# Kernel tuning notes

Hardware: AMD Instinct MI355X
Metric: run time of the kernel (lower is better)

Reference implementation:

```python
import jax, jax.numpy as jnp
import numpy as np

EPS = 0.1        # entropic regularization
MAX_ITER = 50    # max Sinkhorn iterations
THRESH = 0.1     # early-stop threshold on |u - u1|


def setup_inputs() -> dict:
    key = jax.random.key(0)
    kx, ky = jax.random.split(key)
    x = jax.random.normal(kx, (4, 3072, 32), dtype=jnp.float32)
    y = jax.random.normal(ky, (4, 3072, 32), dtype=jnp.float32)
    return {"x": x, "y": y}


def _sinkhorn(x, y):
    B, P1, _ = x.shape
    P2 = y.shape[1]
    x2 = jnp.sum(x * x, axis=-1)                       # [B, P1]
    y2 = jnp.sum(y * y, axis=-1)                       # [B, P2]
    C = x2[:, :, None] + y2[:, None, :] - 2.0 * jnp.einsum('bid,bjd->bij', x, y)  # [B,P1,P2]

    log_mu = jnp.log(jnp.float32(1.0 / P1) + 1e-8)     # uniform marginals
    log_nu = jnp.log(jnp.float32(1.0 / P2) + 1e-8)

    def M(u, v):
        # modified cost M_ij = (-C_ij + u_i + v_j) / eps
        return (-C + u[:, :, None] + v[:, None, :]) / EPS

    def step(carry, _):
        u, v, done = carry
        u_new = EPS * (log_mu - jax.nn.logsumexp(M(u, v), axis=-1)) + u
        v_new = EPS * (log_nu - jax.nn.logsumexp(M(u_new, v), axis=-2)) + v
        err = jnp.mean(jnp.sum(jnp.abs(u_new - u), axis=-1))
        # freeze updates once converged (emulates the torch early break)
        u_out = jnp.where(done, u, u_new)
        v_out = jnp.where(done, v, v_new)
        done = done | (err < THRESH)
        return (u_out, v_out, done), None

    u0 = jnp.zeros((B, P1), dtype=C.dtype)
    v0 = jnp.zeros((B, P2), dtype=C.dtype)
    (u, v, _), _ = jax.lax.scan(jax.checkpoint(step), (u0, v0, jnp.array(False)),
                                None, length=MAX_ITER)

    pi = jnp.exp(M(u, v))                              # transport plan [B,P1,P2]
    cost = jnp.sum(pi * C, axis=(-2, -1))              # [B]  (reduction='none')
    return cost, pi, C


def reference(x, y):
    return _sinkhorn(x, y)
```

## Files before the change

kernel.cpp:

```cpp
#include <hip/hip_runtime.h>
#include <math.h>

#define BATCH 4
#define P 3072
#define NROW (BATCH * P)
#define NTILE (NROW / 16)
#define TPB (P / 16)
#define MAXIT 50
#define LSE_GRID NTILE

#define LN2 0.69314718055994531f
#define INV_LN2 1.44269504088896341f

typedef _Float16 f16x8 __attribute__((ext_vector_type(8)));
typedef float f32x4 __attribute__((ext_vector_type(4)));

__device__ inline float waveReduceSum(float v) {
#pragma unroll
  for (int off = 32; off > 0; off >>= 1) v += __shfl_xor(v, off, 64);
  return v;
}
__device__ inline float fexp2(float x) { return __builtin_amdgcn_exp2f(x); }
__device__ inline float flog2(float x) { return __builtin_amdgcn_logf(x); }

__global__ __launch_bounds__(256) void prep_kernel(const float* __restrict__ x,
                                                   const float* __restrict__ y,
                                                   _Float16* __restrict__ xh,
                                                   _Float16* __restrict__ yh,
                                                   float* __restrict__ x2,
                                                   float* __restrict__ y2,
                                                   float* __restrict__ vb) {
  int t = threadIdx.x;
  int lane = t & 63;
  int g = lane >> 4, r = lane & 15;
  int tileG = blockIdx.x * 4 + (t >> 6);
  int isY = tileG >= NTILE;
  int tile = isY ? (tileG - NTILE) : tileG;
  const float* src = isY ? y : x;
  int row = tile * 16 + r;
  const float* p = src + (size_t)row * 32 + g * 8;
  float4 v0 = *(const float4*)p;
  float4 v1 = *(const float4*)(p + 4);
  float sq = v0.x * v0.x + v0.y * v0.y + v0.z * v0.z + v0.w * v0.w +
             v1.x * v1.x + v1.y * v1.y + v1.z * v1.z + v1.w * v1.w;
  sq += __shfl_xor(sq, 16, 64);
  sq += __shfl_xor(sq, 32, 64);
  float scale = isY ? 1.0f : 20.0f * INV_LN2;
  f16x8 h;
  h[0] = (_Float16)(scale * v0.x); h[1] = (_Float16)(scale * v0.y);
  h[2] = (_Float16)(scale * v0.z); h[3] = (_Float16)(scale * v0.w);
  h[4] = (_Float16)(scale * v1.x); h[5] = (_Float16)(scale * v1.y);
  h[6] = (_Float16)(scale * v1.z); h[7] = (_Float16)(scale * v1.w);
  _Float16* dst = (isY ? yh : xh) + (size_t)tile * 512 + lane * 8;
  *(f16x8*)dst = h;
  if (lane < 16) {
    if (isY) { y2[row] = sq; vb[row] = -10.0f * INV_LN2 * sq; }
    else     { x2[row] = sq; }
  }
}

template <int PASS>
__global__ __launch_bounds__(256) void lse_kernel(const _Float16* __restrict__ A16,
                                                  const _Float16* __restrict__ B16,
                                                  const float* __restrict__ biasIn,
                                                  const float* __restrict__ nrm,
                                                  float* __restrict__ pot,
                                                  float* __restrict__ biasOut,
                                                  float* __restrict__ errpart,
                                                  int* __restrict__ done_arr,
                                                  int it, float lmn) {
  int tid = threadIdx.x;
  if (done_arr[it]) {
    if (PASS == 1 && blockIdx.x == 0 && tid == 0) done_arr[it + 1] = 1;
    return;
  }
  int lane = tid & 63;
  int w = tid >> 6;
  int rsel = lane & 15;
  int b = blockIdx.x / TPB;
  f16x8 afr = *(const f16x8*)(A16 + (size_t)blockIdx.x * 512 + lane * 8);
  int jt0 = b * TPB + w * 48;
  const _Float16* Bp = B16 + (size_t)jt0 * 512 + lane * 8;
  const float* biasp = biasIn + b * P + w * 768 + rsel;
  float m[4], s[4];
#pragma unroll
  for (int r = 0; r < 4; ++r) { m[r] = -1e30f; s[r] = 0.f; }
#pragma unroll 3
  for (int c = 0; c < 12; ++c) {
    f16x8 bfr[4];
    float bb[4];
#pragma unroll
    for (int t4 = 0; t4 < 4; ++t4) {
      bfr[t4] = *(const f16x8*)(Bp + ((size_t)(c * 4 + t4) << 9));
      bb[t4] = biasp[(c * 4 + t4) * 16];
    }
    f32x4 acc[4];
#pragma unroll
    for (int t4 = 0; t4 < 4; ++t4) {
      f32x4 ci = {bb[t4], bb[t4], bb[t4], bb[t4]};
      acc[t4] = __builtin_amdgcn_mfma_f32_16x16x32_f16(afr, bfr[t4], ci, 0, 0, 0);
    }
#pragma unroll
    for (int r = 0; r < 4; ++r) {
      float a0 = acc[0][r], a1 = acc[1][r], a2 = acc[2][r], a3 = acc[3][r];
      float cm = fmaxf(fmaxf(a0, a1), fmaxf(a2, a3));
      float nm = fmaxf(m[r], cm);
      float e = fexp2(a0 - nm) + fexp2(a1 - nm) + fexp2(a2 - nm) + fexp2(a3 - nm);
      s[r] = s[r] * fexp2(m[r] - nm) + e;
      m[r] = nm;
    }
  }
#pragma unroll
  for (int r = 0; r < 4; ++r) {
#pragma unroll
    for (int off = 1; off < 16; off <<= 1) {
      float om = __shfl_xor(m[r], off, 64);
      float os = __shfl_xor(s[r], off, 64);
      float nm = fmaxf(m[r], om);
      s[r] = s[r] * fexp2(m[r] - nm) + os * fexp2(om - nm);
      m[r] = nm;
    }
  }
  __shared__ float lm[4][16], ls[4][16];
  if (rsel == 0) {
    int g = lane >> 4;
#pragma unroll
    for (int r = 0; r < 4; ++r) {
      lm[w][g * 4 + r] = m[r];
      ls[w][g * 4 + r] = s[r];
    }
  }
  __syncthreads();
  float e = 0.f;
  if (tid < 16) {
    float M = lm[0][tid], S = ls[0][tid];
#pragma unroll
    for (int w2 = 1; w2 < 4; ++w2) {
      float om = lm[w2][tid], os = ls[w2][tid];
      float nm = fmaxf(M, om);
      S = S * fexp2(M - nm) + os * fexp2(om - nm);
      M = nm;
    }
    float L2v = M + flog2(S);
    int gi = blockIdx.x * 16 + tid;
    float nv = 0.1f * lmn + nrm[gi] - 0.1f * LN2 * L2v;
    if (PASS == 0) e = fabsf(nv - pot[gi]);
    pot[gi] = nv;
    biasOut[gi] = 10.0f * INV_LN2 * (nv - nrm[gi]);
  }
  if (PASS == 0) {
    if (tid < 64) {
      e = waveReduceSum(e);
      if (tid == 0) errpart[blockIdx.x] = e;
    }
  } else if (blockIdx.x == 0) {
    __shared__ float rr[4];
    float ts = 0.f;
    for (int q = tid; q < LSE_GRID; q += 256) ts += errpart[q];
    ts = waveReduceSum(ts);
    if ((tid & 63) == 0) rr[tid >> 6] = ts;
    __syncthreads();
    if (tid == 0)
      done_arr[it + 1] = ((rr[0] + rr[1] + rr[2] + rr[3]) * 0.25f < 0.1f) ? 1 : 0;
  }
}

__global__ __launch_bounds__(256) void final_kernel(const float* __restrict__ x,
                                                    const float* __restrict__ y,
                                                    const float* __restrict__ x2,
                                                    const float* __restrict__ y2,
                                                    const float* __restrict__ u,
                                                    const float* __restrict__ v,
                                                    float* __restrict__ C,
                                                    float* __restrict__ pi,
                                                    float* __restrict__ costpart) {
  __shared__ float xs[64][33];
  __shared__ float ys[64][33];
  int t = threadIdx.x;
  int b = blockIdx.z;
  int i0 = blockIdx.x * 64;
  int j0 = blockIdx.y * 64;
  const float4* xg = (const float4*)(x + ((size_t)b * P + i0) * 32);
  const float4* yg = (const float4*)(y + ((size_t)b * P + j0) * 32);
#pragma unroll
  for (int k = 0; k < 2; ++k) {
    int f4 = t + k * 256;
    int row = f4 >> 3;
    int col = (f4 & 7) << 2;
    float4 xv = xg[f4];
    xs[row][col] = xv.x; xs[row][col + 1] = xv.y; xs[row][col + 2] = xv.z; xs[row][col + 3] = xv.w;
    float4 yv = yg[f4];
    ys[row][col] = yv.x; ys[row][col + 1] = yv.y; ys[row][col + 2] = yv.z; ys[row][col + 3] = yv.w;
  }
  __syncthreads();
  int ti = t >> 4, tj = t & 15;
  int ib = ti * 4, jb = tj * 4;
  float acc[4][4];
#pragma unroll
  for (int a = 0; a < 4; ++a)
#pragma unroll
    for (int bb = 0; bb < 4; ++bb) acc[a][bb] = 0.f;
#pragma unroll 8
  for (int k = 0; k < 32; ++k) {
    float xa[4], yb[4];
#pragma unroll
    for (int a = 0; a < 4; ++a) xa[a] = xs[ib + a][k];
#pragma unroll
    for (int bb = 0; bb < 4; ++bb) yb[bb] = ys[jb + bb][k];
#pragma unroll
    for (int a = 0; a < 4; ++a)
#pragma unroll
      for (int bb = 0; bb < 4; ++bb) acc[a][bb] = fmaf(xa[a], yb[bb], acc[a][bb]);
  }
  float y2r[4], vr[4];
#pragma unroll
  for (int bb = 0; bb < 4; ++bb) {
    y2r[bb] = y2[b * P + j0 + jb + bb];
    vr[bb] = v[b * P + j0 + jb + bb];
  }
  float costacc = 0.f;
#pragma unroll
  for (int a = 0; a < 4; ++a) {
    int gi = b * P + i0 + ib + a;
    float x2r = x2[gi];
    float ur = u[gi];
    float4 co, po;
    co.x = x2r + y2r[0] - 2.f * acc[a][0];
    co.y = x2r + y2r[1] - 2.f * acc[a][1];
    co.z = x2r + y2r[2] - 2.f * acc[a][2];
    co.w = x2r + y2r[3] - 2.f * acc[a][3];
    po.x = __expf((ur + vr[0] - co.x) * 10.f);
    po.y = __expf((ur + vr[1] - co.y) * 10.f);
    po.z = __expf((ur + vr[2] - co.z) * 10.f);
    po.w = __expf((ur + vr[3] - co.w) * 10.f);
    costacc += po.x * co.x + po.y * co.y + po.z * co.z + po.w * co.w;
    float* crow = C + (size_t)gi * P + j0;
    ((float4*)crow)[tj] = co;
    float* prow = pi + (size_t)gi * P + j0;
    ((float4*)prow)[tj] = po;
  }
  costacc = waveReduceSum(costacc);
  __shared__ float red[4];
  if ((t & 63) == 0) red[t >> 6] = costacc;
  __syncthreads();
  if (t == 0)
    costpart[((size_t)b * 48 + blockIdx.y) * 48 + blockIdx.x] =
        red[0] + red[1] + red[2] + red[3];
}

__global__ __launch_bounds__(256) void cost_kernel(const float* __restrict__ costpart,
                                                   float* __restrict__ cost) {
  __shared__ float red[4];
  int t = threadIdx.x;
  for (int b = 0; b < BATCH; ++b) {
    float loc = 0.f;
    for (int idx = t; idx < 2304; idx += 256) loc += costpart[b * 2304 + idx];
    loc = waveReduceSum(loc);
    if ((t & 63) == 0) red[t >> 6] = loc;
    __syncthreads();
    if (t == 0) cost[b] = red[0] + red[1] + red[2] + red[3];
    __syncthreads();
  }
}

extern "C" void kernel_launch(void* const* d_in, const int* in_sizes, int n_in,
                              void* d_out, int out_size, void* d_ws, size_t ws_size,
                              hipStream_t stream) {
  (void)in_sizes; (void)n_in; (void)out_size; (void)ws_size;
  const float* x = (const float*)d_in[0];
  const float* y = (const float*)d_in[1];
  float* out = (float*)d_out;
  float* cost = out;
  float* pi = out + 4;
  float* C = pi + (size_t)BATCH * P * P;

  float* u = (float*)d_ws;
  int* done_arr = (int*)(u + NROW);
  float* v = (float*)(done_arr + 64);
  float* ub = v + NROW;
  float* vb = ub + NROW;
  float* x2 = vb + NROW;
  float* y2 = x2 + NROW;
  float* errpart = y2 + NROW;
  float* costpart = errpart + LSE_GRID;

  _Float16* xh = (_Float16*)C;
  _Float16* yh = xh + (size_t)NROW * 32;

  hipMemsetAsync(d_ws, 0, (size_t)NROW * sizeof(float) + 64 * sizeof(int), stream);

  float lmn = logf(1.0f / 3072.0f + 1e-8f);

  prep_kernel<<<384, 256, 0, stream>>>(x, y, xh, yh, x2, y2, vb);

  for (int it = 0; it < MAXIT; ++it) {
    lse_kernel<0><<<LSE_GRID, 256, 0, stream>>>(xh, yh, vb, x2, u, ub, errpart,
                                                done_arr, it, lmn);
    lse_kernel<1><<<LSE_GRID, 256, 0, stream>>>(yh, xh, ub, y2, v, vb, errpart,
                                                done_arr, it, lmn);
  }

  final_kernel<<<dim3(48, 48, 4), 256, 0, stream>>>(x, y, x2, y2, u, v, C, pi, costpart);
  cost_kernel<<<1, 256, 0, stream>>>(costpart, cost);
}
```

Measured before the change: 1.702 ms.

## Fuse Sinkhorn iterations into one persistent kernel with grid barriers

Replaces the 100 per-half-iteration kernel launches with a single persistent kernel of 256 blocks of 512 threads that loops over iterations and synchronises with an atomic-counter grid barrier. Each block now owns 48 rows (3 MFMA tiles) and reuses each loaded B fragment across those 3 row tiles. The online logsumexp skips the rescale when no lane's max increases. The aim is to remove launch overhead and early-exit checks per launch. In exchange it depends on all 256 blocks being co-resident, which risks deadlock if they are not, and it adds barrier spin cost each half-step.

After: 3.691 ms. +116.8%, slower.

```diff
diff --git a/kernel.cpp b/kernel.cpp
--- a/kernel.cpp
+++ b/kernel.cpp
@@ -7,7 +7,9 @@
 #define NTILE (NROW / 16)
 #define TPB (P / 16)
 #define MAXIT 50
-#define LSE_GRID NTILE
+#define NBLK 256
+#define RPB 48
+#define CTW 24
 
 #define LN2 0.69314718055994531f
 #define INV_LN2 1.44269504088896341f
@@ -22,6 +24,24 @@
 }
 __device__ inline float fexp2(float x) { return __builtin_amdgcn_exp2f(x); }
 __device__ inline float flog2(float x) { return __builtin_amdgcn_logf(x); }
+
+__device__ inline void gridBarrier(int* cnt, int* gen) {
+  __syncthreads();
+  if (threadIdx.x == 0) {
+    int g = __hip_atomic_load(gen, __ATOMIC_RELAXED, __HIP_MEMORY_SCOPE_AGENT);
+    __threadfence();
+    int a = __hip_atomic_fetch_add(cnt, 1, __ATOMIC_RELAXED, __HIP_MEMORY_SCOPE_AGENT);
+    if (a == NBLK - 1) {
+      __hip_atomic_store(cnt, 0, __ATOMIC_RELAXED, __HIP_MEMORY_SCOPE_AGENT);
+      __hip_atomic_store(gen, g + 1, __ATOMIC_RELAXED, __HIP_MEMORY_SCOPE_AGENT);
+    } else {
+      while (__hip_atomic_load(gen, __ATOMIC_RELAXED, __HIP_MEMORY_SCOPE_AGENT) == g)
+        __builtin_amdgcn_s_sleep(4);
+    }
+    __threadfence();
+  }
+  __syncthreads();
+}
 
 __global__ __launch_bounds__(256) void prep_kernel(const float* __restrict__ x,
                                                    const float* __restrict__ y,
@@ -59,109 +79,141 @@
   }
 }
 
-template <int PASS>
-__global__ __launch_bounds__(256) void lse_kernel(const _Float16* __restrict__ A16,
-                                                  const _Float16* __restrict__ B16,
-                                                  const float* __restrict__ biasIn,
-                                                  const float* __restrict__ nrm,
-                                                  float* __restrict__ pot,
-                                                  float* __restrict__ biasOut,
-                                                  float* __restrict__ errpart,
-                                                  int* __restrict__ done_arr,
-                                                  int it, float lmn) {
+__global__ __launch_bounds__(512, 2) void sinkhorn_kernel(
+    const _Float16* __restrict__ xh, const _Float16* __restrict__ yh,
+    float* __restrict__ u, float* __restrict__ v,
+    float* __restrict__ ub, float* __restrict__ vb,
+    const float* __restrict__ x2, const float* __restrict__ y2,
+    float* __restrict__ errpart, int* __restrict__ bar, float lmn) {
   int tid = threadIdx.x;
-  if (done_arr[it]) {
-    if (PASS == 1 && blockIdx.x == 0 && tid == 0) done_arr[it + 1] = 1;
-    return;
-  }
   int lane = tid & 63;
   int w = tid >> 6;
   int rsel = lane & 15;
-  int b = blockIdx.x / TPB;
-  f16x8 afr = *(const f16x8*)(A16 + (size_t)blockIdx.x * 512 + lane * 8);
-  int jt0 = b * TPB + w * 48;
-  const _Float16* Bp = B16 + (size_t)jt0 * 512 + lane * 8;
-  const float* biasp = biasIn + b * P + w * 768 + rsel;
-  float m[4], s[4];
-#pragma unroll
-  for (int r = 0; r < 4; ++r) { m[r] = -1e30f; s[r] = 0.f; }
-#pragma unroll 3
-  for (int c = 0; c < 12; ++c) {
-    f16x8 bfr[4];
-    float bb[4];
-#pragma unroll
-    for (int t4 = 0; t4 < 4; ++t4) {
-      bfr[t4] = *(const f16x8*)(Bp + ((size_t)(c * 4 + t4) << 9));
-      bb[t4] = biasp[(c * 4 + t4) * 16];
-    }
-    f32x4 acc[4];
-#pragma unroll
-    for (int t4 = 0; t4 < 4; ++t4) {
-      f32x4 ci = {bb[t4], bb[t4], bb[t4], bb[t4]};
-      acc[t4] = __builtin_amdgcn_mfma_f32_16x16x32_f16(afr, bfr[t4], ci, 0, 0, 0);
-    }
-#pragma unroll
-    for (int r = 0; r < 4; ++r) {
-      float a0 = acc[0][r], a1 = acc[1][r], a2 = acc[2][r], a3 = acc[3][r];
-      float cm = fmaxf(fmaxf(a0, a1), fmaxf(a2, a3));
-      float nm = fmaxf(m[r], cm);
-      float e = fexp2(a0 - nm) + fexp2(a1 - nm) + fexp2(a2 - nm) + fexp2(a3 - nm);
-      s[r] = s[r] * fexp2(m[r] - nm) + e;
-      m[r] = nm;
-    }
-  }
-#pragma unroll
-  for (int r = 0; r < 4; ++r) {
-#pragma unroll
-    for (int off = 1; off < 16; off <<= 1) {
-      float om = __shfl_xor(m[r], off, 64);
-      float os = __shfl_xor(s[r], off, 64);
-      float nm = fmaxf(m[r], om);
-      s[r] = s[r] * fexp2(m[r] - nm) + os * fexp2(om - nm);
-      m[r] = nm;
-    }
-  }
-  __shared__ float lm[4][16], ls[4][16];
-  if (rsel == 0) {
-    int g = lane >> 4;
-#pragma unroll
-    for (int r = 0; r < 4; ++r) {
-      lm[w][g * 4 + r] = m[r];
-      ls[w][g * 4 + r] = s[r];
-    }
-  }
-  __syncthreads();
-  float e = 0.f;
-  if (tid < 16) {
-    float M = lm[0][tid], S = ls[0][tid];
-#pragma unroll
-    for (int w2 = 1; w2 < 4; ++w2) {
-      float om = lm[w2][tid], os = ls[w2][tid];
-      float nm = fmaxf(M, om);
-      S = S * fexp2(M - nm) + os * fexp2(om - nm);
-      M = nm;
-    }
-    float L2v = M + flog2(S);
-    int gi = blockIdx.x * 16 + tid;
-    float nv = 0.1f * lmn + nrm[gi] - 0.1f * LN2 * L2v;
-    if (PASS == 0) e = fabsf(nv - pot[gi]);
-    pot[gi] = nv;
-    biasOut[gi] = 10.0f * INV_LN2 * (nv - nrm[gi]);
-  }
-  if (PASS == 0) {
-    if (tid < 64) {
+  int bid = blockIdx.x;
+  int b = bid >> 6;
+  int tile0 = bid * 3;
+  int gr0 = bid * RPB;
+  f16x8 xfr[3], yfr[3];
+#pragma unroll
+  for (int rt = 0; rt < 3; ++rt) {
+    xfr[rt] = *(const f16x8*)(xh + (size_t)(tile0 + rt) * 512 + lane * 8);
+    yfr[rt] = *(const f16x8*)(yh + (size_t)(tile0 + rt) * 512 + lane * 8);
+  }
+  size_t jbase = ((size_t)(b * TPB + w * CTW)) * 512 + lane * 8;
+  const _Float16* BxP = xh + jbase;
+  const _Float16* ByP = yh + jbase;
+  int biasoff = b * P + w * (CTW * 16) + rsel;
+
+  __shared__ float lm[8][RPB], ls[8][RPB];
+  __shared__ int sdone;
+
+  auto halfstep = [&](const f16x8* afr, const _Float16* Bp, const float* biasIn,
+                      const float* nrm, float* pot, float* biasOut, bool trackErr) {
+    const float* biasp = biasIn + biasoff;
+    float m[3][4], s[3][4];
+#pragma unroll
+    for (int rt = 0; rt < 3; ++rt)
+#pragma unroll
+      for (int r = 0; r < 4; ++r) { m[rt][r] = -1e30f; s[rt][r] = 0.f; }
+#pragma unroll 2
+    for (int c = 0; c < 6; ++c) {
+      f16x8 bfr[4];
+      float bb[4];
+#pragma unroll
+      for (int t4 = 0; t4 < 4; ++t4) {
+        bfr[t4] = *(const f16x8*)(Bp + ((size_t)(c * 4 + t4) << 9));
+        bb[t4] = biasp[(c * 4 + t4) * 16];
+      }
+      f32x4 acc[3][4];
+#pragma unroll
+      for (int rt = 0; rt < 3; ++rt)
+#pragma unroll
+        for (int t4 = 0; t4 < 4; ++t4) {
+          f32x4 ci = {bb[t4], bb[t4], bb[t4], bb[t4]};
+          acc[rt][t4] = __builtin_amdgcn_mfma_f32_16x16x32_f16(afr[rt], bfr[t4], ci, 0, 0, 0);
+        }
+#pragma unroll
+      for (int rt = 0; rt < 3; ++rt)
+#pragma unroll
+        for (int r = 0; r < 4; ++r) {
+          float a0 = acc[rt][0][r], a1 = acc[rt][1][r], a2 = acc[rt][2][r], a3 = acc[rt][3][r];
+          float cm = fmaxf(fmaxf(a0, a1), fmaxf(a2, a3));
+          if (__any(cm > m[rt][r])) {
+            float nm = fmaxf(m[rt][r], cm);
+            s[rt][r] = s[rt][r] * fexp2(m[rt][r] - nm) +
+                       fexp2(a0 - nm) + fexp2(a1 - nm) + fexp2(a2 - nm) + fexp2(a3 - nm);
+            m[rt][r] = nm;
+          } else {
+            float mm = m[rt][r];
+            s[rt][r] += fexp2(a0 - mm) + fexp2(a1 - mm) + fexp2(a2 - mm) + fexp2(a3 - mm);
+          }
+        }
+    }
+#pragma unroll
+    for (int rt = 0; rt < 3; ++rt)
+#pragma unroll
+      for (int r = 0; r < 4; ++r) {
+#pragma unroll
+        for (int off = 1; off < 16; off <<= 1) {
+          float om = __shfl_xor(m[rt][r], off, 64);
+          float os = __shfl_xor(s[rt][r], off, 64);
+          float nm = fmaxf(m[rt][r], om);
+          s[rt][r] = s[rt][r] * fexp2(m[rt][r] - nm) + os * fexp2(om - nm);
+          m[rt][r] = nm;
+        }
+      }
+    __syncthreads();
+    if (rsel == 0) {
+      int g = lane >> 4;
+#pragma unroll
+      for (int rt = 0; rt < 3; ++rt)
+#pragma unroll
+        for (int r = 0; r < 4; ++r) {
+          lm[w][rt * 16 + g * 4 + r] = m[rt][r];
+          ls[w][rt * 16 + g * 4 + r] = s[rt][r];
+        }
+    }
+    __syncthreads();
+    float e = 0.f;
+    if (tid < RPB) {
+      float M = lm[0][tid], S = ls[0][tid];
+#pragma unroll
+      for (int w2 = 1; w2 < 8; ++w2) {
+        float om = lm[w2][tid], os = ls[w2][tid];
+        float nm = fmaxf(M, om);
+        S = S * fexp2(M - nm) + os * fexp2(om - nm);
+        M = nm;
+      }
+      float L2v = M + flog2(S);
+      int gi = gr0 + tid;
+      float nv = 0.1f * lmn + nrm[gi] - 0.1f * LN2 * L2v;
+      if (trackErr) e = fabsf(nv - pot[gi]);
+      pot[gi] = nv;
+      biasOut[gi] = 10.0f * INV_LN2 * (nv - nrm[gi]);
+    }
+    if (trackErr && tid < 64) {
       e = waveReduceSum(e);
-      if (tid == 0) errpart[blockIdx.x] = e;
-    }
-  } else if (blockIdx.x == 0) {
-    __shared__ float rr[4];
-    float ts = 0.f;
-    for (int q = tid; q < LSE_GRID; q += 256) ts += errpart[q];
-    ts = waveReduceSum(ts);
-    if ((tid & 63) == 0) rr[tid >> 6] = ts;
-    __syncthreads();
+      if (tid == 0) errpart[bid] = e;
+    }
+  };
+
+  for (int it = 0; it < MAXIT; ++it) {
+    halfstep(xfr, ByP, vb, x2, u, ub, true);
+    gridBarrier(bar, bar + 1);
+    if (bid == 0 && tid < 64) {
+      float ts = errpart[tid] + errpart[tid + 64] +
+                 errpart[tid + 128] + errpart[tid + 192];
+      ts = waveReduceSum(ts);
+      if (tid == 0)
+        __hip_atomic_store(bar + 2, (ts * 0.25f < 0.1f) ? 1 : 0,
+                           __ATOMIC_RELAXED, __HIP_MEMORY_SCOPE_AGENT);
+    }
+    halfstep(yfr, BxP, ub, y2, v, vb, false);
+    gridBarrier(bar, bar + 1);
     if (tid == 0)
-      done_arr[it + 1] = ((rr[0] + rr[1] + rr[2] + rr[3]) * 0.25f < 0.1f) ? 1 : 0;
+      sdone = __hip_atomic_load(bar + 2, __ATOMIC_RELAXED, __HIP_MEMORY_SCOPE_AGENT);
+    __syncthreads();
+    if (sdone) break;
   }
 }
 
@@ -275,14 +327,14 @@
   float* C = pi + (size_t)BATCH * P * P;
 
   float* u = (float*)d_ws;
-  int* done_arr = (int*)(u + NROW);
-  float* v = (float*)(done_arr + 64);
+  int* bar = (int*)(u + NROW);
+  float* v = (float*)(bar + 64);
   float* ub = v + NROW;
   float* vb = ub + NROW;
   float* x2 = vb + NROW;
   float* y2 = x2 + NROW;
   float* errpart = y2 + NROW;
-  float* costpart = errpart + LSE_GRID;
+  float* costpart = errpart + NBLK;
 
   _Float16* xh = (_Float16*)C;
   _Float16* yh = xh + (size_t)NROW * 32;
@@ -292,14 +344,8 @@
   float lmn = logf(1.0f / 3072.0f + 1e-8f);
 
   prep_kernel<<<384, 256, 0, stream>>>(x, y, xh, yh, x2, y2, vb);
-
-  for (int it = 0; it < MAXIT; ++it) {
-    lse_kernel<0><<<LSE_GRID, 256, 0, stream>>>(xh, yh, vb, x2, u, ub, errpart,
-                                                done_arr, it, lmn);
-    lse_kernel<1><<<LSE_GRID, 256, 0, stream>>>(yh, xh, ub, y2, v, vb, errpart,
-                                                done_arr, it, lmn);
-  }
-
+  sinkhorn_kernel<<<NBLK, 512, 0, stream>>>(xh, yh, u, v, ub, vb, x2, y2,
+                                            errpart, bar, lmn);
   final_kernel<<<dim3(48, 48, 4), 256, 0, stream>>>(x, y, x2, y2, u, v, C, pi, costpart);
   cost_kernel<<<1, 256, 0, stream>>>(costpart, cost);
 }
```
